# Optimization experiments

Measured on AMD Instinct MI355X. Metric: run time of the kernel, lower is better.

## Reference

```python
import jax, jax.numpy as jnp
import numpy as np

# Fixed problem sizes (equal-sized batch segments, matching setup_inputs)
B, N, M = 4, 4096, 16384          # clouds, coarse pts/cloud, fine pts/cloud
C_IN, C_SKIP, K = 256, 256, 3     # feature dims, knn k
CH = [C_IN + C_SKIP, 512, 256]    # MLP channels
EPS = 1e-16


def setup_inputs() -> dict:
    key = jax.random.key(0)
    ks = jax.random.split(key, 6)
    x = jax.random.normal(ks[0], (B * N, C_IN), jnp.float32)
    pos = jax.random.uniform(ks[1], (B * N, 3), jnp.float32)
    batch = jnp.repeat(jnp.arange(B, dtype=jnp.int64), N)
    x_skip = jax.random.normal(ks[2], (B * M, C_SKIP), jnp.float32)
    pos_skip = jax.random.uniform(ks[3], (B * M, 3), jnp.float32)
    batch_skip = jnp.repeat(jnp.arange(B, dtype=jnp.int64), M)
    W1 = jax.random.normal(ks[4], (CH[0], CH[1]), jnp.float32) / np.sqrt(CH[0]).astype(np.float32)
    b1 = jnp.zeros((CH[1],), jnp.float32)
    W2 = jax.random.normal(ks[5], (CH[1], CH[2]), jnp.float32) / np.sqrt(CH[1]).astype(np.float32)
    b2 = jnp.zeros((CH[2],), jnp.float32)
    return dict(x=x, pos=pos, batch=batch, x_skip=x_skip, pos_skip=pos_skip,
                batch_skip=batch_skip, W1=W1, b1=b1, W2=W2, b2=b2)


def _knn_interpolate(x, pos, pos_skip):
    """torch_geometric.nn.knn_interpolate with equal-sized batch segments."""
    xb = x.reshape(B, N, C_IN)
    ps = pos.reshape(B, N, 3)
    qs = pos_skip.reshape(B, M, 3)
    # squared pairwise distances [B, M, N]
    d2 = (jnp.sum(qs * qs, -1)[:, :, None]
          - 2.0 * jnp.einsum('bmd,bnd->bmn', qs, ps)
          + jnp.sum(ps * ps, -1)[:, None, :])
    neg_d2, idx = jax.lax.top_k(-d2, K)                # k smallest distances, [B,M,K]
    w = 1.0 / jnp.clip(-neg_d2, EPS)                   # inverse squared distance weights
    feats = jax.vmap(lambda f, i: f[i])(xb, idx)       # gather: [B, M, K, C_IN]
    y = jnp.sum(w[..., None] * feats, axis=2) / jnp.sum(w, axis=2)[..., None]
    return y.reshape(B * M, C_IN)


def reference(x, pos, batch, x_skip, pos_skip, batch_skip, W1, b1, W2, b2):
    y = _knn_interpolate(x, pos, pos_skip)
    h = jnp.concatenate([y, x_skip], axis=1)           # [B*M, 512]
    h = jax.nn.relu(h @ W1 + b1)
    h = jax.nn.relu(h @ W2 + b2)
    return h, pos_skip, batch_skip
```

## Files before the change

### kernel.cpp

```cpp
#include <hip/hip_runtime.h>
#include <stdint.h>

#define NB 4
#define NPTS 4096
#define MPTS 16384
#define CIN 256
#define CH0 512
#define CH1 512
#define CH2 256
#define ROWS (NB * MPTS)
#define POS_OUT_OFF (ROWS * CH2)
#define BATCH_OUT_OFF (POS_OUT_OFF + ROWS * 3)
#define CELL_CAP 40
#define QCAP 96

using u16 = unsigned short;
using u32 = unsigned int;
using u64 = unsigned long long;

typedef __bf16 bf16x8 __attribute__((ext_vector_type(8)));
typedef float f32x4 __attribute__((ext_vector_type(4)));

__device__ __forceinline__ u16 f2bf(float f) {
  u32 u = __builtin_bit_cast(u32, f);
  u32 r = u + 0x7fffu + ((u >> 16) & 1u);
  return (u16)(r >> 16);
}

__device__ __forceinline__ u32 flipf(float f) {
  u32 u = __builtin_bit_cast(u32, f);
  return u ^ ((u32)((int)u >> 31) | 0x80000000u);
}
__device__ __forceinline__ float unflipf(u32 f) {
  u32 m = (~(u32)((int)f >> 31)) | 0x80000000u;
  return __builtin_bit_cast(float, f ^ m);
}

__device__ __forceinline__ void ins3(u64 v, u64& k0, u64& k1, u64& k2) {
  u64 a = k0 < v ? v : k0;
  k0 = k0 < v ? k0 : v;
  u64 bb = k1 < a ? a : k1;
  k1 = k1 < a ? k1 : a;
  k2 = k2 < bb ? k2 : bb;
}

__device__ __forceinline__ void merge3(u64 r0, u64 r1, u64 r2,
                                       u64& k0, u64& k1, u64& k2) {
  u64 t = k0 < r0 ? r0 : k0;
  k0 = k0 < r0 ? k0 : r0;
  u64 u = k1 < r1 ? k1 : r1;
  u64 mtu = t < u ? u : t;
  k1 = t < u ? t : u;
  u64 v = k2 < r2 ? k2 : r2;
  k2 = mtu < v ? mtu : v;
}

__device__ __forceinline__ u64 shfl_xor_u64_w8(u64 v, int mask) {
  u32 lo = (u32)v, hi = (u32)(v >> 32);
  lo = (u32)__shfl_xor((int)lo, mask, 8);
  hi = (u32)__shfl_xor((int)hi, mask, 8);
  return ((u64)hi << 32) | lo;
}

__global__ __launch_bounds__(256) void preptail_kernel(
    const float* __restrict__ W1, const float* __restrict__ W2,
    u16* __restrict__ W1s, u16* __restrict__ W2s,
    const float* __restrict__ pos_skip, const int* __restrict__ batch_skip,
    float* __restrict__ out) {
  const int bid = blockIdx.x;
  if (bid < 192) {
    const int t = bid * 256 + threadIdx.x;
    if (t < 32768) {
      const int l = t & 63, ni = (t >> 6) & 3, wd = (t >> 8) & 7, kt = t >> 11;
      const int fr = l & 15, g = l >> 4;
      const int n = wd * 64 + ni * 16 + fr;
      u16 o[8];
#pragma unroll
      for (int j = 0; j < 8; ++j)
        o[j] = f2bf(W1[(kt * 32 + g * 8 + j) * CH1 + n]);
      *(uint4*)(W1s + (size_t)t * 8) = *(const uint4*)o;
    } else {
      const int c = t - 32768;
      const int l = c & 63, ni = (c >> 6) & 1, wd = (c >> 7) & 7, kt = c >> 10;
      const int fr = l & 15, g = l >> 4;
      const int n = wd * 32 + ni * 16 + fr;
      u16 o[8];
#pragma unroll
      for (int j = 0; j < 8; ++j)
        o[j] = f2bf(W2[(kt * 32 + g * 8 + j) * CH2 + n]);
      *(uint4*)(W2s + (size_t)c * 8) = *(const uint4*)o;
    }
  } else {
    const int t = (bid - 192) * 256 + threadIdx.x;
    if (t < ROWS * 3) {
      out[POS_OUT_OFF + t] = pos_skip[t];
    } else {
      int u = t - ROWS * 3;
      out[BATCH_OUT_OFF + u] = (float)batch_skip[u];
    }
  }
}

__global__ __launch_bounds__(256) void bin_kernel(
    const float* __restrict__ pos, float4* __restrict__ pts4,
    u32* __restrict__ cellCnt, int* __restrict__ cellIdx,
    const float* __restrict__ pos_skip, u32* __restrict__ qCnt,
    int* __restrict__ qIdx) {
#pragma clang fp contract(off)
  if (blockIdx.x < 64) {
    const int i = blockIdx.x * 256 + threadIdx.x;
    const float x = pos[i * 3 + 0], y = pos[i * 3 + 1], z = pos[i * 3 + 2];
    pts4[i] = make_float4(x, y, z, (x * x + y * y) + z * z);
    const int b = i >> 12;
    int cx = (int)(x * 8.0f); cx = cx < 0 ? 0 : (cx > 7 ? 7 : cx);
    int cy = (int)(y * 8.0f); cy = cy < 0 ? 0 : (cy > 7 ? 7 : cy);
    int cz = (int)(z * 8.0f); cz = cz < 0 ? 0 : (cz > 7 ? 7 : cz);
    const int c = b * 512 + cz * 64 + cy * 8 + cx;
    const u32 slot = atomicAdd(&cellCnt[c], 1u);
    if (slot < CELL_CAP) cellIdx[c * CELL_CAP + slot] = i;
  } else {
    const int q = (blockIdx.x - 64) * 256 + threadIdx.x;
    const int b = q >> 14;
    const float qx = pos_skip[q * 3 + 0];
    const float qy = pos_skip[q * 3 + 1];
    const float qz = pos_skip[q * 3 + 2];
    int cx = (int)(qx * 8.0f); cx = cx < 0 ? 0 : (cx > 7 ? 7 : cx);
    int cy = (int)(qy * 8.0f); cy = cy < 0 ? 0 : (cy > 7 ? 7 : cy);
    int cz = (int)(qz * 8.0f); cz = cz < 0 ? 0 : (cz > 7 ? 7 : cz);
    const int c = b * 512 + cz * 64 + cy * 8 + cx;
    const u32 slot = atomicAdd(&qCnt[c], 1u);
    if (slot < QCAP) qIdx[c * QCAP + slot] = q;
  }
}

__global__ __launch_bounds__(256) void knn_kernel(
    const float4* __restrict__ pts4, const u32* __restrict__ cellCnt,
    const int* __restrict__ cellIdx, const u32* __restrict__ qCnt,
    const int* __restrict__ qIdx, const float* __restrict__ pos_skip,
    int* __restrict__ idx_out, float* __restrict__ w_out) {
#pragma clang fp contract(off)
  __shared__ float4 scand[27 * CELL_CAP];
  __shared__ int    scgi[27 * CELL_CAP];
  __shared__ u32    scnt[27];
  __shared__ int    sbase[27];
  __shared__ u32    nCand;
  const int tid = threadIdx.x;
  const int b = blockIdx.x >> 9;
  const int cell = blockIdx.x & 511;
  const int cz = cell >> 6, cy = (cell >> 3) & 7, cx = cell & 7;
  const int x0 = cx > 0 ? cx - 1 : 0, x1 = cx < 7 ? cx + 1 : 7;
  const int y0 = cy > 0 ? cy - 1 : 0, y1 = cy < 7 ? cy + 1 : 7;
  const int z0 = cz > 0 ? cz - 1 : 0, z1 = cz < 7 ? cz + 1 : 7;
  const int nx = x1 - x0 + 1, ny = y1 - y0 + 1, nz = z1 - z0 + 1;
  const int ncells = nx * ny * nz;
  if (tid == 0) nCand = 0;
  if (tid < ncells) {
    const int lz = tid / (nx * ny);
    const int rem = tid - lz * nx * ny;
    const int ly = rem / nx;
    const int lx = rem - ly * nx;
    const int cg = b * 512 + (z0 + lz) * 64 + (y0 + ly) * 8 + (x0 + lx);
    u32 cnt = cellCnt[cg];
    scnt[tid] = cnt > CELL_CAP ? CELL_CAP : cnt;
    sbase[tid] = cg * CELL_CAP;
  }
  __syncthreads();
  const int slots = ncells * CELL_CAP;
  for (int s = tid; s < slots; s += 256) {
    const int ci = s / CELL_CAP;
    const int sl = s - ci * CELL_CAP;
    if ((u32)sl < scnt[ci]) {
      const int gi = cellIdx[sbase[ci] + sl];
      const float4 p = pts4[gi];
      const u32 d = atomicAdd(&nCand, 1u);
      scand[d] = p;
      scgi[d] = gi;
    }
  }
  __syncthreads();
  const int nC = (int)nCand;
  u32 nq = qCnt[b * 512 + cell];
  if (nq > QCAP) nq = QCAP;
  const int qbase = (b * 512 + cell) * QCAP;
  const int g = tid >> 3;
  const int sub = tid & 7;

  for (int r0q = 0; r0q < (int)nq; r0q += 32) {
    const int qslot = r0q + g;
    if (qslot < (int)nq) {
      const int q = qIdx[qbase + qslot];
      const float qx = pos_skip[q * 3 + 0];
      const float qy = pos_skip[q * 3 + 1];
      const float qz = pos_skip[q * 3 + 2];
      const float q2 = (qx * qx + qy * qy) + qz * qz;
      u64 k0 = ~0ull, k1 = ~0ull, k2 = ~0ull;
      for (int s = sub; s < nC; s += 8) {
        const float4 p = scand[s];
        const float dot = fmaf(qz, p.z, fmaf(qy, p.y, qx * p.x));
        const float tv = (q2 - 2.0f * dot) + p.w;
        const u64 key = ((u64)flipf(tv) << 32) | (u32)scgi[s];
        ins3(key, k0, k1, k2);
      }
#pragma unroll
      for (int mask = 1; mask < 8; mask <<= 1) {
        const u64 r0 = shfl_xor_u64_w8(k0, mask);
        const u64 r1 = shfl_xor_u64_w8(k1, mask);
        const u64 r2 = shfl_xor_u64_w8(k2, mask);
        merge3(r0, r1, r2, k0, k1, k2);
      }
      float m2tv = unflipf((u32)(k2 >> 32));
      if (!(m2tv <= 0.015625f - 1e-5f)) {
        k0 = k1 = k2 = ~0ull;
        const int ex0 = cx > 1 ? cx - 2 : 0, ex1 = cx < 6 ? cx + 2 : 7;
        const int ey0 = cy > 1 ? cy - 2 : 0, ey1 = cy < 6 ? cy + 2 : 7;
        const int ez0 = cz > 1 ? cz - 2 : 0, ez1 = cz < 6 ? cz + 2 : 7;
        for (int zz = ez0; zz <= ez1; ++zz)
          for (int yy = ey0; yy <= ey1; ++yy)
            for (int xx = ex0; xx <= ex1; ++xx) {
              const int cg = b * 512 + zz * 64 + yy * 8 + xx;
              u32 cnt = cellCnt[cg];
              if (cnt > CELL_CAP) cnt = CELL_CAP;
              const int cb = cg * CELL_CAP;
              for (int s = sub; s < (int)cnt; s += 8) {
                const int gi = cellIdx[cb + s];
                const float4 p = pts4[gi];
                const float dot = fmaf(qz, p.z, fmaf(qy, p.y, qx * p.x));
                const float tv = (q2 - 2.0f * dot) + p.w;
                ins3(((u64)flipf(tv) << 32) | (u32)gi, k0, k1, k2);
              }
            }
#pragma unroll
        for (int mask = 1; mask < 8; mask <<= 1) {
          const u64 r0 = shfl_xor_u64_w8(k0, mask);
          const u64 r1 = shfl_xor_u64_w8(k1, mask);
          const u64 r2 = shfl_xor_u64_w8(k2, mask);
          merge3(r0, r1, r2, k0, k1, k2);
        }
        m2tv = unflipf((u32)(k2 >> 32));
        if (!(m2tv <= 0.0625f - 1e-5f)) {
          k0 = k1 = k2 = ~0ull;
          const int base = b * NPTS;
          for (int i = sub; i < NPTS; i += 8) {
            const int gi = base + i;
            const float4 p = pts4[gi];
            const float dot = fmaf(qz, p.z, fmaf(qy, p.y, qx * p.x));
            const float tv = (q2 - 2.0f * dot) + p.w;
            ins3(((u64)flipf(tv) << 32) | (u32)gi, k0, k1, k2);
          }
#pragma unroll
          for (int mask = 1; mask < 8; mask <<= 1) {
            const u64 r0 = shfl_xor_u64_w8(k0, mask);
            const u64 r1 = shfl_xor_u64_w8(k1, mask);
            const u64 r2 = shfl_xor_u64_w8(k2, mask);
            merge3(r0, r1, r2, k0, k1, k2);
          }
        }
      }
      if (sub == 0) {
        const float t0 = unflipf((u32)(k0 >> 32));
        const float t1 = unflipf((u32)(k1 >> 32));
        const float t2 = unflipf((u32)(k2 >> 32));
        const float w0 = 1.0f / fmaxf(t0, 1e-16f);
        const float w1 = 1.0f / fmaxf(t1, 1e-16f);
        const float w2 = 1.0f / fmaxf(t2, 1e-16f);
        const float wsum = (w0 + w1) + w2;
        const float inv = 1.0f / wsum;
        idx_out[q * 3 + 0] = (int)(u32)k0;
        idx_out[q * 3 + 1] = (int)(u32)k1;
        idx_out[q * 3 + 2] = (int)(u32)k2;
        w_out[q * 3 + 0] = w0 * inv;
        w_out[q * 3 + 1] = w1 * inv;
        w_out[q * 3 + 2] = w2 * inv;
      }
    }
  }
}

__global__ __launch_bounds__(512, 2) void fused_mlp_kernel(
    const float* __restrict__ x, const int* __restrict__ idx,
    const float* __restrict__ w, const float* __restrict__ x_skip,
    const u16* __restrict__ W1s, const float* __restrict__ b1,
    const u16* __restrict__ W2s, const float* __restrict__ b2,
    float* __restrict__ out) {
  __shared__ __align__(16) u16 Abuf[64 * 512];
  const int tid = threadIdx.x;
  const int m0 = blockIdx.x * 64;

  {
    const int row = tid >> 3;
    const int sub = tid & 7;
    const int gr = m0 + row;
    u16* rowp = Abuf + row * 512;
    const int rx = row & 7;
    const float4* ps = (const float4*)(x_skip + (size_t)gr * CIN + sub * 32);
    float4 sv0 = ps[0], sv1 = ps[1], sv2 = ps[2], sv3 = ps[3];
    float4 sv4 = ps[4], sv5 = ps[5], sv6 = ps[6], sv7 = ps[7];
    const int i0 = idx[gr * 3 + 0], i1 = idx[gr * 3 + 1], i2 = idx[gr * 3 + 2];
    const float w0 = w[gr * 3 + 0], w1 = w[gr * 3 + 1], w2 = w[gr * 3 + 2];
    const float4* p0 = (const float4*)(x + (size_t)i0 * CIN + sub * 32);
    const float4* p1 = (const float4*)(x + (size_t)i1 * CIN + sub * 32);
    const float4* p2 = (const float4*)(x + (size_t)i2 * CIN + sub * 32);
#pragma unroll
    for (int c = 0; c < 4; ++c) {
      const float4 a0 = p0[c * 2], a1 = p1[c * 2], a2 = p2[c * 2];
      const float4 d0 = p0[c * 2 + 1], d1 = p1[c * 2 + 1], d2 = p2[c * 2 + 1];
      u16 o[8];
      o[0] = f2bf(fmaf(w0, a0.x, fmaf(w1, a1.x, w2 * a2.x)));
      o[1] = f2bf(fmaf(w0, a0.y, fmaf(w1, a1.y, w2 * a2.y)));
      o[2] = f2bf(fmaf(w0, a0.z, fmaf(w1, a1.z, w2 * a2.z)));
      o[3] = f2bf(fmaf(w0, a0.w, fmaf(w1, a1.w, w2 * a2.w)));
      o[4] = f2bf(fmaf(w0, d0.x, fmaf(w1, d1.x, w2 * d2.x)));
      o[5] = f2bf(fmaf(w0, d0.y, fmaf(w1, d1.y, w2 * d2.y)));
      o[6] = f2bf(fmaf(w0, d0.z, fmaf(w1, d1.z, w2 * d2.z)));
      o[7] = f2bf(fmaf(w0, d0.w, fmaf(w1, d1.w, w2 * d2.w)));
      const int p = (c << 3) | (sub ^ rx);
      *(uint4*)(rowp + p * 8) = *(const uint4*)o;
    }
    {
      u16 o[8];
      o[0]=f2bf(sv0.x); o[1]=f2bf(sv0.y); o[2]=f2bf(sv0.z); o[3]=f2bf(sv0.w);
      o[4]=f2bf(sv1.x); o[5]=f2bf(sv1.y); o[6]=f2bf(sv1.z); o[7]=f2bf(sv1.w);
      *(uint4*)(rowp + (32 | (0 << 3) | (sub ^ rx)) * 8) = *(const uint4*)o;
      o[0]=f2bf(sv2.x); o[1]=f2bf(sv2.y); o[2]=f2bf(sv2.z); o[3]=f2bf(sv2.w);
      o[4]=f2bf(sv3.x); o[5]=f2bf(sv3.y); o[6]=f2bf(sv3.z); o[7]=f2bf(sv3.w);
      *(uint4*)(rowp + (32 | (1 << 3) | (sub ^ rx)) * 8) = *(const uint4*)o;
      o[0]=f2bf(sv4.x); o[1]=f2bf(sv4.y); o[2]=f2bf(sv4.z); o[3]=f2bf(sv4.w);
      o[4]=f2bf(sv5.x); o[5]=f2bf(sv5.y); o[6]=f2bf(sv5.z); o[7]=f2bf(sv5.w);
      *(uint4*)(rowp + (32 | (2 << 3) | (sub ^ rx)) * 8) = *(const uint4*)o;
      o[0]=f2bf(sv6.x); o[1]=f2bf(sv6.y); o[2]=f2bf(sv6.z); o[3]=f2bf(sv6.w);
      o[4]=f2bf(sv7.x); o[5]=f2bf(sv7.y); o[6]=f2bf(sv7.z); o[7]=f2bf(sv7.w);
      *(uint4*)(rowp + (32 | (3 << 3) | (sub ^ rx)) * 8) = *(const uint4*)o;
    }
  }
  __syncthreads();

  const int wid = tid >> 6;
  const int lane = tid & 63;
  const int fr = lane & 15;
  const int g = lane >> 4;
  const int frx = fr & 7;

  f32x4 acc[4][4];
#pragma unroll
  for (int mi = 0; mi < 4; mi++)
#pragma unroll
    for (int ni = 0; ni < 4; ni++) acc[mi][ni] = (f32x4){0.f, 0.f, 0.f, 0.f};

  {
    const u16* B1 = W1s + wid * 2048 + lane * 8;
    bf16x8 bf[2][4];
#pragma unroll
    for (int ni = 0; ni < 4; ni++)
      bf[0][ni] = *(const bf16x8*)(B1 + ni * 512);
    for (int kt = 0; kt < 16; ++kt) {
      const int cur = kt & 1;
      if (kt < 15) {
        const u16* nb = B1 + (kt + 1) * 16384;
#pragma unroll
        for (int ni = 0; ni < 4; ni++)
          bf[cur ^ 1][ni] = *(const bf16x8*)(nb + ni * 512);
      }
      bf16x8 af[4];
#pragma unroll
      for (int mi = 0; mi < 4; mi++)
        af[mi] = *(const bf16x8*)&Abuf[(mi * 16 + fr) * 512 +
            ((((kt >> 3) << 5) | (g << 3) | ((kt & 7) ^ frx)) * 8)];
#pragma unroll
      for (int mi = 0; mi < 4; mi++)
#pragma unroll
        for (int ni = 0; ni < 4; ni++)
          acc[mi][ni] = __builtin_amdgcn_mfma_f32_16x16x32_bf16(
              af[mi], bf[cur][ni], acc[mi][ni], 0, 0, 0);
    }
  }
  __syncthreads();

  {
    const int wn = wid * 64;
#pragma unroll
    for (int ni = 0; ni < 4; ni++) {
      const int n = wn + ni * 16 + fr;
      const float bb = b1[n];
      const int vg = n >> 3;
      const int nlow = n & 7;
      const int pb = (vg & 32) | ((vg & 3) << 3) | ((vg >> 2) & 7);
#pragma unroll
      for (int mi = 0; mi < 4; mi++) {
#pragma unroll
        for (int r = 0; r < 4; r++) {
          const int m = mi * 16 + g * 4 + r;
          const float v = fmaxf(acc[mi][ni][r] + bb, 0.f);
          Abuf[m * 512 + (pb ^ (m & 7)) * 8 + nlow] = f2bf(v);
        }
      }
    }
  }
  __syncthreads();

  f32x4 acc2[4][2];
#pragma unroll
  for (int mi = 0; mi < 4; mi++)
#pragma unroll
    for (int ni = 0; ni < 2; ni++) acc2[mi][ni] = (f32x4){0.f, 0.f, 0.f, 0.f};

  {
    const u16* B2 = W2s + wid * 1024 + lane * 8;
    bf16x8 bf[2][2];
#pragma unroll
    for (int ni = 0; ni < 2; ni++)
      bf[0][ni] = *(const bf16x8*)(B2 + ni * 512);
    for (int kt = 0; kt < 16; ++kt) {
      const int cur = kt & 1;
      if (kt < 15) {
        const u16* nb = B2 + (kt + 1) * 8192;
#pragma unroll
        for (int ni = 0; ni < 2; ni++)
          bf[cur ^ 1][ni] = *(const bf16x8*)(nb + ni * 512);
      }
      bf16x8 af[4];
#pragma unroll
      for (int mi = 0; mi < 4; mi++)
        af[mi] = *(const bf16x8*)&Abuf[(mi * 16 + fr) * 512 +
            ((((kt >> 3) << 5) | (g << 3) | ((kt & 7) ^ frx)) * 8)];
#pragma unroll
      for (int mi = 0; mi < 4; mi++)
#pragma unroll
        for (int ni = 0; ni < 2; ni++)
          acc2[mi][ni] = __builtin_amdgcn_mfma_f32_16x16x32_bf16(
              af[mi], bf[cur][ni], acc2[mi][ni], 0, 0, 0);
    }
  }

#pragma unroll
  for (int ni = 0; ni < 2; ni++) {
    const int col = wid * 32 + ni * 16 + fr;
    const float bb = b2[col];
#pragma unroll
    for (int mi = 0; mi < 4; mi++) {
#pragma unroll
      for (int r = 0; r < 4; r++) {
        const int rowg = m0 + mi * 16 + g * 4 + r;
        out[(size_t)rowg * CH2 + col] = fmaxf(acc2[mi][ni][r] + bb, 0.f);
      }
    }
  }
}

extern "C" void kernel_launch(void* const* d_in, const int* in_sizes, int n_in,
                              void* d_out, int out_size, void* d_ws, size_t ws_size,
                              hipStream_t stream) {
  const float* x        = (const float*)d_in[0];
  const float* pos      = (const float*)d_in[1];
  const float* x_skip   = (const float*)d_in[3];
  const float* pos_skip = (const float*)d_in[4];
  const int*   batch_sk = (const int*)d_in[5];
  const float* W1       = (const float*)d_in[6];
  const float* b1       = (const float*)d_in[7];
  const float* W2       = (const float*)d_in[8];
  const float* b2       = (const float*)d_in[9];
  float* out = (float*)d_out;

  char* ws = (char*)d_ws;
  u16*    W1s     = (u16*)(ws);
  u16*    W2s     = (u16*)(ws + 524288);
  int*    idxb    = (int*)(ws + 786432);
  float*  wb      = (float*)(ws + 1572864);
  float4* pts4    = (float4*)(ws + 2359296);
  u32*    cellCnt = (u32*)(ws + 2621440);
  u32*    qCnt    = (u32*)(ws + 2629632);
  int*    cellIdx = (int*)(ws + 2637824);
  int*    qIdx    = (int*)(ws + 2965504);

  hipMemsetAsync(cellCnt, 0, 16384, stream);
  preptail_kernel<<<dim3(1216), dim3(256), 0, stream>>>(
      W1, W2, W1s, W2s, pos_skip, batch_sk, out);
  bin_kernel<<<dim3(320), dim3(256), 0, stream>>>(
      pos, pts4, cellCnt, cellIdx, pos_skip, qCnt, qIdx);
  knn_kernel<<<dim3(2048), dim3(256), 0, stream>>>(pts4, cellCnt, cellIdx,
                                                   qCnt, qIdx, pos_skip,
                                                   idxb, wb);
  fused_mlp_kernel<<<dim3(1024), dim3(512), 0, stream>>>(
      x, idxb, wb, x_skip, W1s, b1, W2s, b2, out);
}
```

Baseline: 270.0 us.

## Process MLP rows in spatial-cell order to improve gather locality

```diff
diff --git a/kernel.cpp b/kernel.cpp
--- a/kernel.cpp
+++ b/kernel.cpp
@@ -131,6 +131,30 @@
     const u32 slot = atomicAdd(&qCnt[c], 1u);
     if (slot < QCAP) qIdx[c * QCAP + slot] = q;
   }
+}
+
+__global__ __launch_bounds__(512) void qperm_kernel(
+    const u32* __restrict__ qCnt, const int* __restrict__ qIdx,
+    int* __restrict__ qPerm) {
+  __shared__ u32 ssc[512];
+  const int b = blockIdx.x;
+  const int tid = threadIdx.x;
+  u32 cnt = qCnt[b * 512 + tid];
+  if (cnt > QCAP) cnt = QCAP;
+  u32 run = cnt;
+  ssc[tid] = run;
+  for (int off = 1; off < 512; off <<= 1) {
+    __syncthreads();
+    u32 t = (tid >= off) ? ssc[tid - off] : 0u;
+    __syncthreads();
+    run += t;
+    ssc[tid] = run;
+  }
+  const u32 excl = run - cnt;
+  const int base = b * MPTS + (int)excl;
+  const int src = (b * 512 + tid) * QCAP;
+  for (u32 j = 0; j < cnt; ++j)
+    qPerm[base + j] = qIdx[src + j];
 }
 
 __global__ __launch_bounds__(256) void knn_kernel(
@@ -281,55 +305,54 @@
     const float* __restrict__ w, const float* __restrict__ x_skip,
     const u16* __restrict__ W1s, const float* __restrict__ b1,
     const u16* __restrict__ W2s, const float* __restrict__ b2,
-    float* __restrict__ out) {
+    const int* __restrict__ qPerm, float* __restrict__ out) {
   __shared__ __align__(16) u16 Abuf[64 * 512];
+  __shared__ int sPerm[64];
   const int tid = threadIdx.x;
   const int m0 = blockIdx.x * 64;
+
+  if (tid < 64) sPerm[tid] = qPerm[m0 + tid];
 
   {
     const int row = tid >> 3;
     const int sub = tid & 7;
-    const int gr = m0 + row;
+    const int gr = qPerm[m0 + row];
     u16* rowp = Abuf + row * 512;
     const int rx = row & 7;
-    const float4* ps = (const float4*)(x_skip + (size_t)gr * CIN + sub * 32);
-    float4 sv0 = ps[0], sv1 = ps[1], sv2 = ps[2], sv3 = ps[3];
-    float4 sv4 = ps[4], sv5 = ps[5], sv6 = ps[6], sv7 = ps[7];
-    const int i0 = idx[gr * 3 + 0], i1 = idx[gr * 3 + 1], i2 = idx[gr * 3 + 2];
-    const float w0 = w[gr * 3 + 0], w1 = w[gr * 3 + 1], w2 = w[gr * 3 + 2];
-    const float4* p0 = (const float4*)(x + (size_t)i0 * CIN + sub * 32);
-    const float4* p1 = (const float4*)(x + (size_t)i1 * CIN + sub * 32);
-    const float4* p2 = (const float4*)(x + (size_t)i2 * CIN + sub * 32);
-#pragma unroll
-    for (int c = 0; c < 4; ++c) {
-      const float4 a0 = p0[c * 2], a1 = p1[c * 2], a2 = p2[c * 2];
-      const float4 d0 = p0[c * 2 + 1], d1 = p1[c * 2 + 1], d2 = p2[c * 2 + 1];
-      u16 o[8];
-      o[0] = f2bf(fmaf(w0, a0.x, fmaf(w1, a1.x, w2 * a2.x)));
-      o[1] = f2bf(fmaf(w0, a0.y, fmaf(w1, a1.y, w2 * a2.y)));
-      o[2] = f2bf(fmaf(w0, a0.z, fmaf(w1, a1.z, w2 * a2.z)));
-      o[3] = f2bf(fmaf(w0, a0.w, fmaf(w1, a1.w, w2 * a2.w)));
-      o[4] = f2bf(fmaf(w0, d0.x, fmaf(w1, d1.x, w2 * d2.x)));
-      o[5] = f2bf(fmaf(w0, d0.y, fmaf(w1, d1.y, w2 * d2.y)));
-      o[6] = f2bf(fmaf(w0, d0.z, fmaf(w1, d1.z, w2 * d2.z)));
-      o[7] = f2bf(fmaf(w0, d0.w, fmaf(w1, d1.w, w2 * d2.w)));
-      const int p = (c << 3) | (sub ^ rx);
-      *(uint4*)(rowp + p * 8) = *(const uint4*)o;
-    }
-    {
-      u16 o[8];
-      o[0]=f2bf(sv0.x); o[1]=f2bf(sv0.y); o[2]=f2bf(sv0.z); o[3]=f2bf(sv0.w);
-      o[4]=f2bf(sv1.x); o[5]=f2bf(sv1.y); o[6]=f2bf(sv1.z); o[7]=f2bf(sv1.w);
-      *(uint4*)(rowp + (32 | (0 << 3) | (sub ^ rx)) * 8) = *(const uint4*)o;
-      o[0]=f2bf(sv2.x); o[1]=f2bf(sv2.y); o[2]=f2bf(sv2.z); o[3]=f2bf(sv2.w);
-      o[4]=f2bf(sv3.x); o[5]=f2bf(sv3.y); o[6]=f2bf(sv3.z); o[7]=f2bf(sv3.w);
-      *(uint4*)(rowp + (32 | (1 << 3) | (sub ^ rx)) * 8) = *(const uint4*)o;
-      o[0]=f2bf(sv4.x); o[1]=f2bf(sv4.y); o[2]=f2bf(sv4.z); o[3]=f2bf(sv4.w);
-      o[4]=f2bf(sv5.x); o[5]=f2bf(sv5.y); o[6]=f2bf(sv5.z); o[7]=f2bf(sv5.w);
-      *(uint4*)(rowp + (32 | (2 << 3) | (sub ^ rx)) * 8) = *(const uint4*)o;
-      o[0]=f2bf(sv6.x); o[1]=f2bf(sv6.y); o[2]=f2bf(sv6.z); o[3]=f2bf(sv6.w);
-      o[4]=f2bf(sv7.x); o[5]=f2bf(sv7.y); o[6]=f2bf(sv7.z); o[7]=f2bf(sv7.w);
-      *(uint4*)(rowp + (32 | (3 << 3) | (sub ^ rx)) * 8) = *(const uint4*)o;
+    if (sub < 4) {
+      const int i0 = idx[gr * 3 + 0], i1 = idx[gr * 3 + 1], i2 = idx[gr * 3 + 2];
+      const float w0 = w[gr * 3 + 0], w1 = w[gr * 3 + 1], w2 = w[gr * 3 + 2];
+      const float4* p0 = (const float4*)(x + (size_t)i0 * CIN + sub * 64);
+      const float4* p1 = (const float4*)(x + (size_t)i1 * CIN + sub * 64);
+      const float4* p2 = (const float4*)(x + (size_t)i2 * CIN + sub * 64);
+#pragma unroll
+      for (int c = 0; c < 8; ++c) {
+        const float4 a0 = p0[c * 2], a1 = p1[c * 2], a2 = p2[c * 2];
+        const float4 d0 = p0[c * 2 + 1], d1 = p1[c * 2 + 1], d2 = p2[c * 2 + 1];
+        u16 o[8];
+        o[0] = f2bf(fmaf(w0, a0.x, fmaf(w1, a1.x, w2 * a2.x)));
+        o[1] = f2bf(fmaf(w0, a0.y, fmaf(w1, a1.y, w2 * a2.y)));
+        o[2] = f2bf(fmaf(w0, a0.z, fmaf(w1, a1.z, w2 * a2.z)));
+        o[3] = f2bf(fmaf(w0, a0.w, fmaf(w1, a1.w, w2 * a2.w)));
+        o[4] = f2bf(fmaf(w0, d0.x, fmaf(w1, d1.x, w2 * d2.x)));
+        o[5] = f2bf(fmaf(w0, d0.y, fmaf(w1, d1.y, w2 * d2.y)));
+        o[6] = f2bf(fmaf(w0, d0.z, fmaf(w1, d1.z, w2 * d2.z)));
+        o[7] = f2bf(fmaf(w0, d0.w, fmaf(w1, d1.w, w2 * d2.w)));
+        const int p = ((c & 3) << 3) | (((2 * sub + (c >> 2)) ^ rx) & 7);
+        *(uint4*)(rowp + p * 8) = *(const uint4*)o;
+      }
+    } else {
+      const int ss = sub - 4;
+      const float4* ps = (const float4*)(x_skip + (size_t)gr * CIN + ss * 64);
+#pragma unroll
+      for (int c = 0; c < 8; ++c) {
+        const float4 a = ps[c * 2], d = ps[c * 2 + 1];
+        u16 o[8];
+        o[0] = f2bf(a.x); o[1] = f2bf(a.y); o[2] = f2bf(a.z); o[3] = f2bf(a.w);
+        o[4] = f2bf(d.x); o[5] = f2bf(d.y); o[6] = f2bf(d.z); o[7] = f2bf(d.w);
+        const int p = 32 | ((c & 3) << 3) | (((2 * ss + (c >> 2)) ^ rx) & 7);
+        *(uint4*)(rowp + p * 8) = *(const uint4*)o;
+      }
     }
   }
   __syncthreads();
@@ -439,7 +462,7 @@
     for (int mi = 0; mi < 4; mi++) {
 #pragma unroll
       for (int r = 0; r < 4; r++) {
-        const int rowg = m0 + mi * 16 + g * 4 + r;
+        const int rowg = sPerm[mi * 16 + g * 4 + r];
         out[(size_t)rowg * CH2 + col] = fmaxf(acc2[mi][ni][r] + bb, 0.f);
       }
     }
@@ -470,15 +493,17 @@
   u32*    qCnt    = (u32*)(ws + 2629632);
   int*    cellIdx = (int*)(ws + 2637824);
   int*    qIdx    = (int*)(ws + 2965504);
+  int*    qPerm   = (int*)(ws + 3751936);
 
   hipMemsetAsync(cellCnt, 0, 16384, stream);
   preptail_kernel<<<dim3(1216), dim3(256), 0, stream>>>(
       W1, W2, W1s, W2s, pos_skip, batch_sk, out);
   bin_kernel<<<dim3(320), dim3(256), 0, stream>>>(
       pos, pts4, cellCnt, cellIdx, pos_skip, qCnt, qIdx);
+  qperm_kernel<<<dim3(4), dim3(512), 0, stream>>>(qCnt, qIdx, qPerm);
   knn_kernel<<<dim3(2048), dim3(256), 0, stream>>>(pts4, cellCnt, cellIdx,
                                                    qCnt, qIdx, pos_skip,
                                                    idxb, wb);
   fused_mlp_kernel<<<dim3(1024), dim3(512), 0, stream>>>(
-      x, idxb, wb, x_skip, W1s, b1, W2s, b2, out);
-}
+      x, idxb, wb, x_skip, W1s, b1, W2s, b2, qPerm, out);
+}
```

After: 267.3 us. No clear change (-1.0%).
